# Kernel optimization log

Hardware: AMD Instinct MI355X
Metric: run time of the kernel (lower is better)

The kernel has to match this reference:

```python
import jax, jax.numpy as jnp
import numpy as np

# irreps layout: list of (multiplicity, l); input == hidden == 128x0e+64x1e+32x2e
IRREPS = [(128, 0), (64, 1), (32, 2)]
EPS = 1e-5


def _split(x, irreps):
    """Split flat [N, dim] into per-irrep fields [N, mul, 2l+1]."""
    fields, ix = [], 0
    for mul, l in irreps:
        d = 2 * l + 1
        fields.append(x[:, ix:ix + mul * d].reshape(-1, mul, d))
        ix += mul * d
    return fields


def _equiv_layernorm(x, w, b):
    """Equivariant layer norm (Equiformer-style): per-irrep RMS over (mul, comp),
    mean-subtraction + bias only for scalars; affine weight per multiplicity."""
    outs, iw = [], 0
    for (mul, l), f in zip(IRREPS, _split(x, IRREPS)):
        if l == 0:
            f = f - f.mean(axis=1, keepdims=True)
        norm2 = (f * f).sum(-1).mean(axis=1)          # [N]
        inv = jax.lax.rsqrt(norm2 + EPS)              # [N]
        f = f * (inv[:, None] * w[iw:iw + mul][None, :])[:, :, None]
        if l == 0:
            f = f + b[None, :, None]
        iw += mul
        outs.append(f.reshape(f.shape[0], -1))
    return jnp.concatenate(outs, axis=1)


def _o3_linear(fields, Ws):
    """Per-irrep linear with e3nn path normalization 1/sqrt(fan_in)."""
    return [jnp.einsum('nui,uv->nvi', f, W) / np.float32(np.sqrt(f.shape[1]))
            for f, W in zip(fields, Ws)]


def _gate(fields):
    """XequiNet Gate: sigmoid of per-channel invariant norm multiplies the channel."""
    out = []
    for f in fields:
        n = jnp.sqrt((f * f).sum(-1) + 1e-12)         # [N, mul]
        out.append(f * jax.nn.sigmoid(n)[..., None])
    return out


def setup_inputs() -> dict:
    key = jax.random.key(0)
    ks = jax.random.split(key, 8)
    N, B = 300000, 512
    atom_out = jax.random.normal(ks[0], (N, 480), dtype=jnp.float32)
    coords = jax.random.normal(ks[1], (N, 3), dtype=jnp.float32)
    at_no = jax.random.randint(ks[2], (N,), 0, 100, dtype=jnp.int64)
    batch_idx = jnp.sort(jax.random.randint(ks[3], (N,), 0, B, dtype=jnp.int64))
    return {
        'atom_out': atom_out,
        'coords': coords,
        'ln_w': jnp.ones((224,), jnp.float32),
        'ln_b': jnp.zeros((128,), jnp.float32),
        'W1_0': jax.random.normal(ks[4], (128, 128), dtype=jnp.float32),
        'W1_1': jax.random.normal(ks[5], (64, 64), dtype=jnp.float32),
        'W1_2': jax.random.normal(ks[6], (32, 32), dtype=jnp.float32),
        'W2': jax.random.normal(ks[7], (64, 1), dtype=jnp.float32),
        'at_no': at_no,
        'batch_idx': batch_idx,
        'num_graphs': B,
    }


def reference(atom_out, coords, ln_w, ln_b, W1_0, W1_1, W1_2, W2, at_no, batch_idx, num_graphs):
    x = _equiv_layernorm(atom_out, ln_w, ln_b)
    fields = _split(x, IRREPS)
    fields = _o3_linear(fields, [W1_0, W1_1, W1_2])
    fields = _gate(fields)
    # second o3.Linear to 1x1e: only the 1e block contributes
    vec = jnp.einsum('nui,uv->nvi', fields[1], W2) / np.float32(np.sqrt(64.0))  # [N,1,3]
    atom_res = vec[:, 0, :][:, jnp.array([2, 0, 1])]  # e3nn (y,z,x) -> (x,y,z)
    return jax.ops.segment_sum(atom_res, batch_idx, num_segments=num_graphs)
```

## Files before the change

kernel.cpp:

```cpp
#include <hip/hip_runtime.h>
#include <hip/hip_bf16.h>

#define WPB 4
#define BLOCK (WPB * 64)
#define GRID 512

typedef __attribute__((ext_vector_type(8))) short s16x8;
typedef __attribute__((ext_vector_type(4))) float f32x4;

__device__ __forceinline__ float wave_sum64(float v) {
#pragma unroll
    for (int m = 32; m >= 1; m >>= 1) v += __shfl_xor(v, m, 64);
    return v;
}

__device__ __forceinline__ short bf16b(float x) {
    union { float f; unsigned u; } c; c.f = x;
    unsigned r = c.u + 0x7FFFu + ((c.u >> 16) & 1u);
    return (short)(r >> 16);
}

__global__ __launch_bounds__(BLOCK, 2) void vecout_mfma(
    const float* __restrict__ atom_out,
    const float* __restrict__ ln_w,
    const float* __restrict__ W1_1,
    const float* __restrict__ W2,
    const int*   __restrict__ batch_idx,
    float* __restrict__ out,
    int N)
{
    __shared__ __align__(16) short Ash[WPB][48 * 64];
    __shared__ float invsh[WPB][16];

    const int lane  = threadIdx.x & 63;
    const int wid   = threadIdx.x >> 6;
    const int col   = lane & 15;
    const int kgrp  = lane >> 4;
    const int atomi = lane & 15;
    const unsigned swz = (unsigned)(lane & 7) << 4;

    const int NG = (N + 15) >> 4;
    const int NW = gridDim.x * WPB;
    const int w  = blockIdx.x * WPB + wid;
    const int cpw = NG / NW, rem = NG % NW;
    const int g0  = w * cpw + min(w, rem);
    const int cnt = cpw + (w < rem ? 1 : 0);
    if (cnt <= 0) return;
    const int gend = g0 + cnt;

    s16x8 Bf[2][4];
#pragma unroll
    for (int kt = 0; kt < 2; ++kt)
#pragma unroll
        for (int nt = 0; nt < 4; ++nt) {
            s16x8 b;
#pragma unroll
            for (int j = 0; j < 8; ++j) {
                int k = kt * 32 + kgrp * 8 + j;
                float wgt = W1_1[k * 64 + nt * 16 + col] * ln_w[128 + k] * 0.125f;
                b[j] = bf16b(wgt);
            }
            Bf[kt][nt] = b;
        }
    float w2r[4];
#pragma unroll
    for (int nt = 0; nt < 4; ++nt) w2r[nt] = W2[nt * 16 + col] * 0.125f;

    char* Ab = (char*)(&Ash[wid][0]);

    float acc[4][3];
#pragma unroll
    for (int r = 0; r < 4; ++r) { acc[r][0] = 0.f; acc[r][1] = 0.f; acc[r][2] = 0.f; }
    int accb = batch_idx[g0 * 16];

    auto flushAcc = [&]() {
        float s0 = acc[0][0] + acc[1][0] + acc[2][0] + acc[3][0];
        float s1 = acc[0][1] + acc[1][1] + acc[2][1] + acc[3][1];
        float s2 = acc[0][2] + acc[1][2] + acc[2][2] + acc[3][2];
        s0 = wave_sum64(s0); s1 = wave_sum64(s1); s2 = wave_sum64(s2);
        if (lane == 0) {
            atomicAdd(&out[accb * 3 + 0], s2);
            atomicAdd(&out[accb * 3 + 1], s0);
            atomicAdd(&out[accb * 3 + 2], s1);
        }
#pragma unroll
        for (int r = 0; r < 4; ++r) { acc[r][0] = 0.f; acc[r][1] = 0.f; acc[r][2] = 0.f; }
    };

    auto loadG = [&](float (&R)[48], int g) {
        int myatom = g * 16 + atomi;
        int ma = min(myatom, N - 1);
        const float4* p = reinterpret_cast<const float4*>(
            atom_out + (size_t)ma * 480 + 128 + kgrp * 48);
#pragma unroll
        for (int j = 0; j < 12; ++j) {
            float4 t = p[j];
            R[4 * j + 0] = t.x; R[4 * j + 1] = t.y;
            R[4 * j + 2] = t.z; R[4 * j + 3] = t.w;
        }
    };

    auto computeG = [&](const float (&R)[48], int g) {
        int a = g * 16;

        float nrm = 0.f;
#pragma unroll
        for (int m = 0; m < 48; ++m) nrm += R[m] * R[m];
        nrm += __shfl_xor(nrm, 16, 64);
        nrm += __shfl_xor(nrm, 32, 64);
        float inv = rsqrtf(nrm * (1.0f / 64.0f) + 1e-5f);
        if (lane < 16) invsh[wid][lane] = inv;

#pragma unroll
        for (int c = 0; c < 3; ++c) {
            s16x8 P0, P1;
#pragma unroll
            for (int j = 0; j < 8; ++j) P0[j] = bf16b(R[3 * j + c]);
#pragma unroll
            for (int j = 0; j < 8; ++j) P1[j] = bf16b(R[3 * (j + 8) + c]);
            unsigned rr = (unsigned)(c * 16 + atomi) * 128u;
            unsigned ub = (unsigned)kgrp * 32u;
            *(s16x8*)(Ab + rr + (ub ^ swz))         = P0;
            *(s16x8*)(Ab + rr + ((ub + 16u) ^ swz)) = P1;
        }
        asm volatile("s_waitcnt lgkmcnt(0)" ::: "memory");

        s16x8 Af[3][2];
#pragma unroll
        for (int c = 0; c < 3; ++c)
#pragma unroll
            for (int kt = 0; kt < 2; ++kt) {
                unsigned rr = (unsigned)(c * 16 + atomi) * 128u;
                unsigned ub = (unsigned)(kt * 64 + kgrp * 16);
                Af[c][kt] = *(const s16x8*)(Ab + rr + (ub ^ swz));
            }

        f32x4 Cf[3][4];
#pragma unroll
        for (int c = 0; c < 3; ++c)
#pragma unroll
            for (int nt = 0; nt < 4; ++nt) {
                f32x4 z = {0.f, 0.f, 0.f, 0.f};
                z = __builtin_amdgcn_mfma_f32_16x16x32_bf16(Af[c][0], Bf[0][nt], z, 0, 0, 0);
                z = __builtin_amdgcn_mfma_f32_16x16x32_bf16(Af[c][1], Bf[1][nt], z, 0, 0, 0);
                Cf[c][nt] = z;
            }

        float invA[4];
#pragma unroll
        for (int r = 0; r < 4; ++r) invA[r] = invsh[wid][kgrp * 4 + r];

        float part[4][3];
#pragma unroll
        for (int r = 0; r < 4; ++r) {
            part[r][0] = 0.f; part[r][1] = 0.f; part[r][2] = 0.f;
            float iv = invA[r];
#pragma unroll
            for (int nt = 0; nt < 4; ++nt) {
                float g0v = Cf[0][nt][r] * iv;
                float g1v = Cf[1][nt][r] * iv;
                float g2v = Cf[2][nt][r] * iv;
                float q  = g0v * g0v + g1v * g1v + g2v * g2v;
                float nr = sqrtf(q + 1e-12f);
                float sg = 1.f / (1.f + __expf(-nr));
                float t  = sg * w2r[nt];
                part[r][0] += g0v * t; part[r][1] += g1v * t; part[r][2] += g2v * t;
            }
            if (a + kgrp * 4 + r >= N) { part[r][0] = 0.f; part[r][1] = 0.f; part[r][2] = 0.f; }
        }

        int bfst = batch_idx[a];
        int blst = batch_idx[min(a + 15, N - 1)];
        if (bfst == blst) {
            if (bfst != accb) { flushAcc(); accb = bfst; }
#pragma unroll
            for (int r = 0; r < 4; ++r) {
                acc[r][0] += part[r][0]; acc[r][1] += part[r][1]; acc[r][2] += part[r][2];
            }
        } else {
            flushAcc();
#pragma unroll
            for (int r = 0; r < 4; ++r) {
                float c0 = part[r][0], c1 = part[r][1], c2 = part[r][2];
#pragma unroll
                for (int m = 1; m < 16; m <<= 1) {
                    c0 += __shfl_xor(c0, m, 64);
                    c1 += __shfl_xor(c1, m, 64);
                    c2 += __shfl_xor(c2, m, 64);
                }
                int ai = a + kgrp * 4 + r;
                if (col == 0 && ai < N) {
                    int b = batch_idx[ai];
                    atomicAdd(&out[b * 3 + 0], c2);
                    atomicAdd(&out[b * 3 + 1], c0);
                    atomicAdd(&out[b * 3 + 2], c1);
                }
            }
            accb = blst;
        }
    };

    float RA[48], RB[48];
    int g = g0;
    loadG(RA, g);
    while (true) {
        int gn = g + 1;
        if (gn < gend) loadG(RB, gn);
        computeG(RA, g);
        if (gn >= gend) break;
        g = gn; gn = g + 1;
        if (gn < gend) loadG(RA, gn);
        computeG(RB, g);
        if (gn >= gend) break;
        g = gn;
    }

    flushAcc();
}

extern "C" void kernel_launch(void* const* d_in, const int* in_sizes, int n_in,
                              void* d_out, int out_size, void* d_ws, size_t ws_size,
                              hipStream_t stream) {
    const float* atom_out  = (const float*)d_in[0];
    const float* ln_w      = (const float*)d_in[2];
    const float* W1_1      = (const float*)d_in[5];
    const float* W2        = (const float*)d_in[7];
    const int*   batch_idx = (const int*)d_in[9];
    float* out = (float*)d_out;

    const int N = in_sizes[0] / 480;

    hipMemsetAsync(d_out, 0, (size_t)out_size * sizeof(float), stream);

    vecout_mfma<<<GRID, BLOCK, 0, stream>>>(atom_out, ln_w, W1_1, W2, batch_idx, out, N);
}
```

Baseline: 68.00 us.

## Stream atom tiles via global_load_lds with swizzled LDS and single-buffer prefetch

Replaces the register double-buffered float4 loads with direct global-to-LDS async loads (global_load_lds, 16 bytes per lane) into a swizzled per-wave LDS tile. The next tile is prefetched after the current tile has been read out of LDS. The bf16 A fragments are now built directly in registers, with no LDS round trip. Freeing the 96 prefetch registers allows raising occupancy to 3 blocks per SM with a larger grid, at the cost of more LDS per block and a full vmcnt wait each iteration.

New measurement: 72.37 us. 1.06x slower.

```diff
diff --git a/kernel.cpp b/kernel.cpp
--- a/kernel.cpp
+++ b/kernel.cpp
@@ -3,10 +3,14 @@
 
 #define WPB 4
 #define BLOCK (WPB * 64)
-#define GRID 512
+#define GRID 768
 
 typedef __attribute__((ext_vector_type(8))) short s16x8;
 typedef __attribute__((ext_vector_type(4))) float f32x4;
+
+#define GLL16(gp, lp) __builtin_amdgcn_global_load_lds( \
+    (const __attribute__((address_space(1))) void*)(gp), \
+    (__attribute__((address_space(3))) void*)(lp), 16, 0, 0)
 
 __device__ __forceinline__ float wave_sum64(float v) {
 #pragma unroll
@@ -20,7 +24,7 @@
     return (short)(r >> 16);
 }
 
-__global__ __launch_bounds__(BLOCK, 2) void vecout_mfma(
+__global__ __launch_bounds__(BLOCK, 3) void vecout_mfma(
     const float* __restrict__ atom_out,
     const float* __restrict__ ln_w,
     const float* __restrict__ W1_1,
@@ -29,7 +33,7 @@
     float* __restrict__ out,
     int N)
 {
-    __shared__ __align__(16) short Ash[WPB][48 * 64];
+    __shared__ __align__(16) char Ash[WPB][12288];
     __shared__ float invsh[WPB][16];
 
     const int lane  = threadIdx.x & 63;
@@ -37,11 +41,10 @@
     const int col   = lane & 15;
     const int kgrp  = lane >> 4;
     const int atomi = lane & 15;
-    const unsigned swz = (unsigned)(lane & 7) << 4;
-
-    const int NG = (N + 15) >> 4;
-    const int NW = gridDim.x * WPB;
-    const int w  = blockIdx.x * WPB + wid;
+
+    const int NG  = (N + 15) >> 4;
+    const int NW  = gridDim.x * WPB;
+    const int w   = blockIdx.x * WPB + wid;
     const int cpw = NG / NW, rem = NG % NW;
     const int g0  = w * cpw + min(w, rem);
     const int cnt = cpw + (w < rem ? 1 : 0);
@@ -66,7 +69,20 @@
 #pragma unroll
     for (int nt = 0; nt < 4; ++nt) w2r[nt] = W2[nt * 16 + col] * 0.125f;
 
-    char* Ab = (char*)(&Ash[wid][0]);
+    int prec[12];
+#pragma unroll
+    for (int c = 0; c < 12; ++c) {
+        int P   = c * 1024 + lane * 16;
+        int row = P / 768;
+        int L   = P ^ ((row & 7) << 4);
+        prec[c] = row * 1920 + 512 + (L - row * 768);
+    }
+
+    const char* gb = (const char*)atom_out;
+    char* Ab = &Ash[wid][0];
+
+    const unsigned key   = (unsigned)(atomi & 7) << 4;
+    const unsigned base0 = (unsigned)(atomi * 768 + kgrp * 96);
 
     float acc[4][3];
 #pragma unroll
@@ -87,52 +103,62 @@
         for (int r = 0; r < 4; ++r) { acc[r][0] = 0.f; acc[r][1] = 0.f; acc[r][2] = 0.f; }
     };
 
-    auto loadG = [&](float (&R)[48], int g) {
-        int myatom = g * 16 + atomi;
-        int ma = min(myatom, N - 1);
-        const float4* p = reinterpret_cast<const float4*>(
-            atom_out + (size_t)ma * 480 + 128 + kgrp * 48);
-#pragma unroll
-        for (int j = 0; j < 12; ++j) {
-            float4 t = p[j];
-            R[4 * j + 0] = t.x; R[4 * j + 1] = t.y;
-            R[4 * j + 2] = t.z; R[4 * j + 3] = t.w;
+    auto issueG = [&](int g) {
+        if (((g + 1) << 4) <= N) {
+            const char* p = gb + (size_t)g * 30720;
+#pragma unroll
+            for (int c = 0; c < 12; ++c)
+                GLL16(p + prec[c], Ab + c * 1024);
+        } else {
+#pragma unroll
+            for (int c = 0; c < 12; ++c) {
+                int P   = c * 1024 + lane * 16;
+                int row = P / 768;
+                int off = (P ^ ((row & 7) << 4)) - row * 768;
+                int ga  = min(g * 16 + row, N - 1);
+                GLL16(gb + (size_t)ga * 1920 + 512 + off, Ab + c * 1024);
+            }
         }
     };
 
-    auto computeG = [&](const float (&R)[48], int g) {
+    issueG(g0);
+
+    for (int g = g0; g < gend; ++g) {
         int a = g * 16;
 
+        asm volatile("s_waitcnt vmcnt(0)" ::: "memory");
+
+        float F[48];
+#pragma unroll
+        for (int kt = 0; kt < 2; ++kt)
+#pragma unroll
+            for (int s = 0; s < 6; ++s) {
+                unsigned ad = (base0 + (unsigned)(kt * 384 + s * 16)) ^ key;
+                f32x4 t = *(const f32x4*)(Ab + ad);
+                int i = (kt * 6 + s) * 4;
+                F[i + 0] = t[0]; F[i + 1] = t[1]; F[i + 2] = t[2]; F[i + 3] = t[3];
+            }
+        asm volatile("s_waitcnt lgkmcnt(0)" ::: "memory");
+
+        if (g + 1 < gend) issueG(g + 1);
+
         float nrm = 0.f;
 #pragma unroll
-        for (int m = 0; m < 48; ++m) nrm += R[m] * R[m];
+        for (int i = 0; i < 48; ++i) nrm += F[i] * F[i];
         nrm += __shfl_xor(nrm, 16, 64);
         nrm += __shfl_xor(nrm, 32, 64);
         float inv = rsqrtf(nrm * (1.0f / 64.0f) + 1e-5f);
         if (lane < 16) invsh[wid][lane] = inv;
 
-#pragma unroll
-        for (int c = 0; c < 3; ++c) {
-            s16x8 P0, P1;
-#pragma unroll
-            for (int j = 0; j < 8; ++j) P0[j] = bf16b(R[3 * j + c]);
-#pragma unroll
-            for (int j = 0; j < 8; ++j) P1[j] = bf16b(R[3 * (j + 8) + c]);
-            unsigned rr = (unsigned)(c * 16 + atomi) * 128u;
-            unsigned ub = (unsigned)kgrp * 32u;
-            *(s16x8*)(Ab + rr + (ub ^ swz))         = P0;
-            *(s16x8*)(Ab + rr + ((ub + 16u) ^ swz)) = P1;
-        }
-        asm volatile("s_waitcnt lgkmcnt(0)" ::: "memory");
-
         s16x8 Af[3][2];
 #pragma unroll
         for (int c = 0; c < 3; ++c)
 #pragma unroll
             for (int kt = 0; kt < 2; ++kt) {
-                unsigned rr = (unsigned)(c * 16 + atomi) * 128u;
-                unsigned ub = (unsigned)(kt * 64 + kgrp * 16);
-                Af[c][kt] = *(const s16x8*)(Ab + rr + (ub ^ swz));
+                s16x8 fr;
+#pragma unroll
+                for (int j = 0; j < 8; ++j) fr[j] = bf16b(F[kt * 24 + 3 * j + c]);
+                Af[c][kt] = fr;
             }
 
         f32x4 Cf[3][4];
@@ -198,21 +224,6 @@
             }
             accb = blst;
         }
-    };
-
-    float RA[48], RB[48];
-    int g = g0;
-    loadG(RA, g);
-    while (true) {
-        int gn = g + 1;
-        if (gn < gend) loadG(RB, gn);
-        computeG(RA, g);
-        if (gn >= gend) break;
-        g = gn; gn = g + 1;
-        if (gn < gend) loadG(RA, gn);
-        computeG(RB, g);
-        if (gn >= gend) break;
-        g = gn;
     }
 
     flushAcc();
```

## Load MFMA A-fragments directly from global, dropping the LDS transpose

Applied to the files above, without the earlier changes.

Each lane now loads the 1e-block elements of its atom in a K ordering that matches the MFMA A-fragment layout, so the bf16 fragments are built in registers without the LDS write/read round trip. The per-atom inverse norms are shared with shuffles instead of through shared memory. Loads become nontemporal, batch_idx reads use wave-uniform indices, and MFMAs are interleaved per output tile with the gate epilogue to reduce live accumulator registers. This removes LDS traffic and its wait, at the cost of a less contiguous per-lane load pattern.

Measured after the change: 131.1 us. 1.93x slower.

```diff
diff --git a/kernel.cpp b/kernel.cpp
--- a/kernel.cpp
+++ b/kernel.cpp
@@ -29,19 +29,14 @@
     float* __restrict__ out,
     int N)
 {
-    __shared__ __align__(16) short Ash[WPB][48 * 64];
-    __shared__ float invsh[WPB][16];
-
     const int lane  = threadIdx.x & 63;
-    const int wid   = threadIdx.x >> 6;
     const int col   = lane & 15;
     const int kgrp  = lane >> 4;
     const int atomi = lane & 15;
-    const unsigned swz = (unsigned)(lane & 7) << 4;
-
-    const int NG = (N + 15) >> 4;
-    const int NW = gridDim.x * WPB;
-    const int w  = blockIdx.x * WPB + wid;
+
+    const int NG  = (N + 15) >> 4;
+    const int NW  = gridDim.x * WPB;
+    const int w   = blockIdx.x * WPB + (threadIdx.x >> 6);
     const int cpw = NG / NW, rem = NG % NW;
     const int g0  = w * cpw + min(w, rem);
     const int cnt = cpw + (w < rem ? 1 : 0);
@@ -66,12 +61,10 @@
 #pragma unroll
     for (int nt = 0; nt < 4; ++nt) w2r[nt] = W2[nt * 16 + col] * 0.125f;
 
-    char* Ab = (char*)(&Ash[wid][0]);
-
     float acc[4][3];
 #pragma unroll
     for (int r = 0; r < 4; ++r) { acc[r][0] = 0.f; acc[r][1] = 0.f; acc[r][2] = 0.f; }
-    int accb = batch_idx[g0 * 16];
+    int accb = batch_idx[__builtin_amdgcn_readfirstlane(g0 * 16)];
 
     auto flushAcc = [&]() {
         float s0 = acc[0][0] + acc[1][0] + acc[2][0] + acc[3][0];
@@ -87,90 +80,78 @@
         for (int r = 0; r < 4; ++r) { acc[r][0] = 0.f; acc[r][1] = 0.f; acc[r][2] = 0.f; }
     };
 
-    auto loadG = [&](float (&R)[48], int g) {
-        int myatom = g * 16 + atomi;
-        int ma = min(myatom, N - 1);
-        const float4* p = reinterpret_cast<const float4*>(
-            atom_out + (size_t)ma * 480 + 128 + kgrp * 48);
-#pragma unroll
-        for (int j = 0; j < 12; ++j) {
-            float4 t = p[j];
-            R[4 * j + 0] = t.x; R[4 * j + 1] = t.y;
-            R[4 * j + 2] = t.z; R[4 * j + 3] = t.w;
+    auto loadG = [&](float (&F)[48], int g) {
+        int ma = min(g * 16 + atomi, N - 1);
+        const char* rowp = (const char*)(atom_out + (size_t)ma * 480 + 128)
+                         + kgrp * 96;
+#pragma unroll
+        for (int kt = 0; kt < 2; ++kt) {
+            const f32x4* p = reinterpret_cast<const f32x4*>(rowp + kt * 384);
+#pragma unroll
+            for (int s = 0; s < 6; ++s) {
+                f32x4 t = __builtin_nontemporal_load(&p[s]);
+                int i = kt * 24 + s * 4;
+                F[i + 0] = t[0]; F[i + 1] = t[1];
+                F[i + 2] = t[2]; F[i + 3] = t[3];
+            }
         }
     };
 
-    auto computeG = [&](const float (&R)[48], int g) {
-        int a = g * 16;
+    auto computeG = [&](const float (&F)[48], int g) {
+        const int a = g * 16;
 
         float nrm = 0.f;
 #pragma unroll
-        for (int m = 0; m < 48; ++m) nrm += R[m] * R[m];
+        for (int i = 0; i < 48; ++i) nrm += F[i] * F[i];
         nrm += __shfl_xor(nrm, 16, 64);
         nrm += __shfl_xor(nrm, 32, 64);
         float inv = rsqrtf(nrm * (1.0f / 64.0f) + 1e-5f);
-        if (lane < 16) invsh[wid][lane] = inv;
-
-#pragma unroll
-        for (int c = 0; c < 3; ++c) {
-            s16x8 P0, P1;
-#pragma unroll
-            for (int j = 0; j < 8; ++j) P0[j] = bf16b(R[3 * j + c]);
-#pragma unroll
-            for (int j = 0; j < 8; ++j) P1[j] = bf16b(R[3 * (j + 8) + c]);
-            unsigned rr = (unsigned)(c * 16 + atomi) * 128u;
-            unsigned ub = (unsigned)kgrp * 32u;
-            *(s16x8*)(Ab + rr + (ub ^ swz))         = P0;
-            *(s16x8*)(Ab + rr + ((ub + 16u) ^ swz)) = P1;
-        }
-        asm volatile("s_waitcnt lgkmcnt(0)" ::: "memory");
+        float invA[4];
+#pragma unroll
+        for (int r = 0; r < 4; ++r) invA[r] = __shfl(inv, kgrp * 4 + r, 64);
 
         s16x8 Af[3][2];
 #pragma unroll
         for (int c = 0; c < 3; ++c)
 #pragma unroll
             for (int kt = 0; kt < 2; ++kt) {
-                unsigned rr = (unsigned)(c * 16 + atomi) * 128u;
-                unsigned ub = (unsigned)(kt * 64 + kgrp * 16);
-                Af[c][kt] = *(const s16x8*)(Ab + rr + (ub ^ swz));
-            }
-
-        f32x4 Cf[3][4];
-#pragma unroll
-        for (int c = 0; c < 3; ++c)
-#pragma unroll
-            for (int nt = 0; nt < 4; ++nt) {
-                f32x4 z = {0.f, 0.f, 0.f, 0.f};
-                z = __builtin_amdgcn_mfma_f32_16x16x32_bf16(Af[c][0], Bf[0][nt], z, 0, 0, 0);
-                z = __builtin_amdgcn_mfma_f32_16x16x32_bf16(Af[c][1], Bf[1][nt], z, 0, 0, 0);
-                Cf[c][nt] = z;
-            }
-
-        float invA[4];
-#pragma unroll
-        for (int r = 0; r < 4; ++r) invA[r] = invsh[wid][kgrp * 4 + r];
+                s16x8 fr;
+#pragma unroll
+                for (int j = 0; j < 8; ++j) fr[j] = bf16b(F[kt * 24 + 3 * j + c]);
+                Af[c][kt] = fr;
+            }
 
         float part[4][3];
 #pragma unroll
-        for (int r = 0; r < 4; ++r) {
-            part[r][0] = 0.f; part[r][1] = 0.f; part[r][2] = 0.f;
-            float iv = invA[r];
-#pragma unroll
-            for (int nt = 0; nt < 4; ++nt) {
-                float g0v = Cf[0][nt][r] * iv;
-                float g1v = Cf[1][nt][r] * iv;
-                float g2v = Cf[2][nt][r] * iv;
+        for (int r = 0; r < 4; ++r) { part[r][0] = 0.f; part[r][1] = 0.f; part[r][2] = 0.f; }
+#pragma unroll
+        for (int nt = 0; nt < 4; ++nt) {
+            f32x4 C0 = {0.f,0.f,0.f,0.f}, C1 = {0.f,0.f,0.f,0.f}, C2 = {0.f,0.f,0.f,0.f};
+            C0 = __builtin_amdgcn_mfma_f32_16x16x32_bf16(Af[0][0], Bf[0][nt], C0, 0, 0, 0);
+            C0 = __builtin_amdgcn_mfma_f32_16x16x32_bf16(Af[0][1], Bf[1][nt], C0, 0, 0, 0);
+            C1 = __builtin_amdgcn_mfma_f32_16x16x32_bf16(Af[1][0], Bf[0][nt], C1, 0, 0, 0);
+            C1 = __builtin_amdgcn_mfma_f32_16x16x32_bf16(Af[1][1], Bf[1][nt], C1, 0, 0, 0);
+            C2 = __builtin_amdgcn_mfma_f32_16x16x32_bf16(Af[2][0], Bf[0][nt], C2, 0, 0, 0);
+            C2 = __builtin_amdgcn_mfma_f32_16x16x32_bf16(Af[2][1], Bf[1][nt], C2, 0, 0, 0);
+#pragma unroll
+            for (int r = 0; r < 4; ++r) {
+                float iv  = invA[r];
+                float g0v = C0[r] * iv;
+                float g1v = C1[r] * iv;
+                float g2v = C2[r] * iv;
                 float q  = g0v * g0v + g1v * g1v + g2v * g2v;
                 float nr = sqrtf(q + 1e-12f);
                 float sg = 1.f / (1.f + __expf(-nr));
                 float t  = sg * w2r[nt];
                 part[r][0] += g0v * t; part[r][1] += g1v * t; part[r][2] += g2v * t;
             }
+        }
+#pragma unroll
+        for (int r = 0; r < 4; ++r)
             if (a + kgrp * 4 + r >= N) { part[r][0] = 0.f; part[r][1] = 0.f; part[r][2] = 0.f; }
-        }
-
-        int bfst = batch_idx[a];
-        int blst = batch_idx[min(a + 15, N - 1)];
+
+        int bfst = batch_idx[__builtin_amdgcn_readfirstlane(a)];
+        int blst = batch_idx[__builtin_amdgcn_readfirstlane(min(a + 15, N - 1))];
         if (bfst == blst) {
             if (bfst != accb) { flushAcc(); accb = bfst; }
 #pragma unroll
@@ -230,7 +211,7 @@
 
     const int N = in_sizes[0] / 480;
 
-    hipMemsetAsync(d_out, 0, (size_t)out_size * sizeof(float), stream);
+    (void)hipMemsetAsync(d_out, 0, (size_t)out_size * sizeof(float), stream);
 
     vecout_mfma<<<GRID, BLOCK, 0, stream>>>(atom_out, ln_w, W1_1, W2, batch_idx, out, N);
 }
```
